# Performance work log

Hardware: AMD Instinct MI355X
Metric: run time of the kernel (lower is better)

The kernel has to match this reference:

```python
import jax, jax.numpy as jnp
import numpy as np

B, T, C, HEAD = 4, 4096, 1024, 64

def _rope_tables(t, d):
    # standard RoPE angles; each frequency repeated for the (even, odd) pair
    inv_freq = 1.0 / (10000.0 ** (np.arange(0, d, 2, dtype=np.float32) / d))  # (d/2,)
    ang = np.arange(t, dtype=np.float32)[:, None] * inv_freq[None, :]          # (t, d/2)
    ang = np.repeat(ang, 2, axis=-1)                                           # (t, d)
    return jnp.asarray(np.cos(ang)), jnp.asarray(np.sin(ang))

def setup_inputs() -> dict:
    key = jax.random.key(0)
    kx, kq, kk, kv = jax.random.split(key, 4)
    cos, sin = _rope_tables(T, HEAD)
    s = 1.0 / np.sqrt(C)
    return {
        "x": jax.random.normal(kx, (B, T, C), dtype=jnp.float32),
        "cos": cos,
        "sin": sin,
        "tril": jnp.tril(jnp.ones((T, T), dtype=jnp.int32)),
        "Wq": jax.random.normal(kq, (C, HEAD), dtype=jnp.float32) * s,
        "Wk": jax.random.normal(kk, (C, HEAD), dtype=jnp.float32) * s,
        "Wv": jax.random.normal(kv, (C, HEAD), dtype=jnp.float32) * s,
    }

def _apply_rope(x, cos, sin):
    # x: (B, T, D); cos/sin: (T, D)
    x1 = x[..., ::2]
    x2 = x[..., 1::2]
    rot = jnp.stack([-x2, x1], axis=-1).reshape(x.shape)
    return x * cos[None] + rot * sin[None]

def reference(x, cos, sin, tril, Wq, Wk, Wv):
    q = _apply_rope(x @ Wq, cos, sin)          # (B, T, D)
    k = _apply_rope(x @ Wk, cos, sin)          # (B, T, D)
    v = x @ Wv                                  # (B, T, D)
    scale = HEAD ** -0.5
    wei = jnp.einsum("btd,bsd->bts", q, k) * scale   # (B, T, T)
    wei = jnp.where(tril[None] == 0, -jnp.inf, wei)
    wei = jax.nn.softmax(wei, axis=-1)               # dropout p=0 (eval) -> identity
    return jnp.einsum("bts,bsd->btd", wei, v)        # (B, T, D)
```

## Files before the change

### kernel.cpp

```cpp
#include <hip/hip_runtime.h>
#include <math.h>

#define T_ 4096
#define NROWS 16384

typedef __attribute__((ext_vector_type(8))) short short8;
typedef __attribute__((ext_vector_type(4))) short short4v;
typedef __attribute__((ext_vector_type(4))) float float4v;
typedef __attribute__((ext_vector_type(2))) unsigned uint2v;

#define MFMA(a, b, c) __builtin_amdgcn_mfma_f32_16x16x32_bf16((a), (b), (c), 0, 0, 0)

#if defined(__has_builtin)
#if __has_builtin(__builtin_amdgcn_exp2f)
#define EXP2(x) __builtin_amdgcn_exp2f(x)
#else
#define EXP2(x) exp2f(x)
#endif
#else
#define EXP2(x) exp2f(x)
#endif

#define SCALE_Q 0.18033688011112042f

__device__ __forceinline__ short f2bf(float f) {
    unsigned u = __builtin_bit_cast(unsigned, f);
    u += 0x7fffu + ((u >> 16) & 1u);
    return (short)(u >> 16);
}
__device__ __forceinline__ float bf2f(short s) {
    return __builtin_bit_cast(float, ((unsigned)(unsigned short)s) << 16);
}
__device__ __forceinline__ unsigned pack_bf2(float a, float b) {
    unsigned ua = __builtin_bit_cast(unsigned, a);
    unsigned ub = __builtin_bit_cast(unsigned, b);
    ua += 0x7fffu + ((ua >> 16) & 1u);
    ub += 0x7fffu + ((ub >> 16) & 1u);
    return (ua >> 16) | (ub & 0xffff0000u);
}

__global__ void wprep_kernel(const float* __restrict__ Wq,
                             const float* __restrict__ Wk,
                             const float* __restrict__ Wv,
                             short* __restrict__ Wt2)
{
    const int ck = blockIdx.x;
    const int t = threadIdx.x;
    const int sub = t >> 6, lane = t & 63;
    const int ln = lane & 15, quad = lane >> 4;
#pragma unroll
    for (int jj = 0; jj < 3; ++jj) {
        const int nt = sub * 3 + jj;
        const float* W = (nt < 4) ? Wq : (nt < 8) ? Wk : Wv;
        const int col = (nt & 3) * 16 + ln;
        short8 o;
#pragma unroll
        for (int j = 0; j < 8; ++j)
            o[j] = f2bf(W[(size_t)(ck * 32 + quad * 8 + j) * 64 + col]);
        *(short8*)(Wt2 + ((size_t)(ck * 12 + nt) * 64 + lane) * 8) = o;
    }
}

__global__ __launch_bounds__(256, 2) void qkv_kernel(
    const float* __restrict__ x, const float* __restrict__ cosp,
    const float* __restrict__ sinp, const short* __restrict__ Wt2,
    short* __restrict__ Qb, short* __restrict__ Ks, short* __restrict__ Vs)
{
    __shared__ short4v MB[4][2][12][64];
    __shared__ short KT[32][72];

    const int t = threadIdx.x, w = t >> 6, lane = t & 63;
    const int ln = lane & 15, quad = lane >> 4;
    const int rb = blockIdx.x * 32;
    const int k0 = w * 256;

    const float* xp0 = x + (size_t)(rb + ln) * 1024 + k0 + quad * 8;
    const float* xp1 = x + (size_t)(rb + 16 + ln) * 1024 + k0 + quad * 8;
    const short* wp2 = Wt2 + ((size_t)(w * 8) * 12 * 64 + lane) * 8;

    short8 a[2][8];
#pragma unroll
    for (int af = 0; af < 2; ++af) {
        const float* xp = af ? xp1 : xp0;
        float4 xf[16];
#pragma unroll
        for (int it = 0; it < 8; ++it) {
            xf[it * 2]     = *(const float4*)(xp + it * 32);
            xf[it * 2 + 1] = *(const float4*)(xp + it * 32 + 4);
        }
#pragma unroll
        for (int it = 0; it < 8; ++it) {
            short8 v;
            v[0] = f2bf(xf[it * 2].x);     v[1] = f2bf(xf[it * 2].y);
            v[2] = f2bf(xf[it * 2].z);     v[3] = f2bf(xf[it * 2].w);
            v[4] = f2bf(xf[it * 2 + 1].x); v[5] = f2bf(xf[it * 2 + 1].y);
            v[6] = f2bf(xf[it * 2 + 1].z); v[7] = f2bf(xf[it * 2 + 1].w);
            a[af][it] = v;
        }
    }

    float4v acc[2][12];
#pragma unroll
    for (int af = 0; af < 2; ++af)
#pragma unroll
        for (int i = 0; i < 12; ++i) acc[af][i] = (float4v){0.f, 0.f, 0.f, 0.f};

#pragma unroll
    for (int it = 0; it < 8; ++it) {
        short8 bf[12];
#pragma unroll
        for (int nt = 0; nt < 12; ++nt)
            bf[nt] = *(const short8*)(wp2 + (size_t)(it * 12 + nt) * 512);
#pragma unroll
        for (int nt = 0; nt < 12; ++nt) {
            acc[0][nt] = MFMA(a[0][it], bf[nt], acc[0][nt]);
            acc[1][nt] = MFMA(a[1][it], bf[nt], acc[1][nt]);
        }
    }

#pragma unroll
    for (int af = 0; af < 2; ++af)
#pragma unroll
        for (int nt = 0; nt < 12; ++nt) {
            short4v pv;
#pragma unroll
            for (int reg = 0; reg < 4; ++reg) pv[reg] = f2bf(acc[af][nt][reg]);
            MB[w][af][nt][lane] = pv;
        }
    __syncthreads();

    const int b  = rb >> 12;
    const int kt = (rb & (T_ - 1)) >> 6;
#pragma unroll
    for (int af = 0; af < 2; ++af) {
        const int rb16 = rb + af * 16;
#pragma unroll
        for (int j = 0; j < 3; ++j) {
            const int nt = w * 3 + j;
            float m[4] = {0.f, 0.f, 0.f, 0.f};
#pragma unroll
            for (int p = 0; p < 4; ++p) {
                const short4v pv = MB[p][af][nt][lane];
#pragma unroll
                for (int reg = 0; reg < 4; ++reg) m[reg] += bf2f(pv[reg]);
            }
            if (nt < 4) {
                const int col = nt * 16 + ln;
#pragma unroll
                for (int reg = 0; reg < 4; ++reg) {
                    const int g  = rb16 + quad * 4 + reg;
                    const int tp = g & (T_ - 1);
                    const float cv = cosp[(size_t)tp * 64 + col];
                    const float sv = sinp[(size_t)tp * 64 + col];
                    const float v  = m[reg];
                    const float vp = __shfl_xor(v, 1, 64);
                    const float rot = (ln & 1) ? vp : -vp;
                    Qb[(size_t)g * 64 + col] = f2bf(fmaf(v, cv, rot * sv) * SCALE_Q);
                }
            } else if (nt < 8) {
                const int col = (nt & 3) * 16 + ln;
#pragma unroll
                for (int reg = 0; reg < 4; ++reg) {
                    const int g  = rb16 + quad * 4 + reg;
                    const int tp = g & (T_ - 1);
                    const float cv = cosp[(size_t)tp * 64 + col];
                    const float sv = sinp[(size_t)tp * 64 + col];
                    const float v  = m[reg];
                    const float vp = __shfl_xor(v, 1, 64);
                    const float rot = (ln & 1) ? vp : -vp;
                    KT[af * 16 + quad * 4 + reg][col] = f2bf(fmaf(v, cv, rot * sv));
                }
            } else {
                const int vnt = nt - 8;
                const int rowgrp = (rb16 >> 4) & 3;
                const int hh = rowgrp >> 1;
                const int qp = (rowgrp & 1) * 2 + (quad >> 1);
                const int jb = (quad & 1) * 4;
                short4v pv;
#pragma unroll
                for (int reg = 0; reg < 4; ++reg) pv[reg] = f2bf(m[reg]);
                const size_t addr =
                    ((((size_t)(b * 64 + kt) * 4 + vnt) * 2 + hh) * 64 + qp * 16 + ln) * 8 + jb;
                *(short4v*)(Vs + addr) = pv;
            }
        }
    }
    __syncthreads();

    {
        const int af2 = w >> 1, h2 = w & 1;
        const int st2 = ((rb >> 4) & 3) + af2;
        const short8 kfrag = *(const short8*)(&KT[af2 * 16 + ln][h2 * 32 + quad * 8]);
        *(short8*)(Ks + (((size_t)(b * 64 + kt) * 8 + st2 * 2 + h2) * 64 + lane) * 8) = kfrag;
    }
}

#define LOADK(kf, ktv)                                                         \
    {   const short* _kb = Ksp + (size_t)(ktv) * 4096 + lane * 8;              \
        _Pragma("unroll")                                                      \
        for (int u = 0; u < 8; ++u) kf[u] = *(const short8*)(_kb + u * 512); }

#define LOADV(vf, ktv)                                                         \
    {   const short* _vb = Vp + (size_t)(ktv) * 4096 + lane * 8;               \
        _Pragma("unroll")                                                      \
        for (int u = 0; u < 8; ++u) vf[u] = *(const short8*)(_vb + u * 512); }

#define CVTPK(dst, lo, hi)                                                     \
    asm("v_cvt_pk_bf16_f32 %0, %1, %2" : "=v"(dst) : "v"(lo), "v"(hi));

#define STEP(ktv, kf, vf, masked)                                              \
    {   float4v sA[4], sB[4];                                                  \
        __builtin_amdgcn_s_setprio(1);                                         \
        _Pragma("unroll")                                                      \
        for (int st = 0; st < 4; ++st) {                                       \
            sA[st] = (float4v){0.f, 0.f, 0.f, 0.f};                            \
            sA[st] = MFMA(kf[st * 2],     qA0, sA[st]);       \
            sA[st] = MFMA(kf[st * 2 + 1], qA1, sA[st]);                        \
            sB[st] = (float4v){0.f, 0.f, 0.f, 0.f};                            \
            sB[st] = MFMA(kf[st * 2],     qB0, sB[st]);                        \
            sB[st] = MFMA(kf[st * 2 + 1], qB1, sB[st]);                        \
        }                                                                      \
        __builtin_amdgcn_s_setprio(0);                                         \
        if (masked) {                                                          \
            _Pragma("unroll")                                                  \
            for (int st = 0; st < 4; ++st)                                     \
                _Pragma("unroll")                                              \
                for (int r = 0; r < 4; ++r) {                                  \
                    const int kc = (ktv) * 64 + st * 16 + quad * 4 + r;        \
                    if (kc > qr0 + ln)      sA[st][r] = -__builtin_inff();     \
                    if (kc > qr0 + 16 + ln) sB[st][r] = -__builtin_inff();     \
                }                                                              \
        }                                                                      \
        _Pragma("unroll")                                                      \
        for (int st = 0; st < 4; ++st)                                         \
            _Pragma("unroll")                                                  \
            for (int r = 0; r < 4; ++r) {                                      \
                const float pA = EXP2(sA[st][r]);                              \
                sA[st][r] = pA; lsumA += pA;                                   \
                const float pB = EXP2(sB[st][r]);                              \
                sB[st][r] = pB; lsumB += pB;                                   \
            }                                                                  \
        _Pragma("unroll")                                                      \
        for (int st = 0; st < 4; ++st) {                                       \
            uint2v pkA, pkB;                                                   \
            CVTPK(pkA[0], sA[st][0], sA[st][1])                                \
            CVTPK(pkA[1], sA[st][2], sA[st][3])                                \
            *(uint2v*)(pwA + ln * 104 + st * 16 + quad * 4) = pkA;             \
            CVTPK(pkB[0], sB[st][0], sB[st][1])                                \
            CVTPK(pkB[1], sB[st][2], sB[st][3])                                \
            *(uint2v*)(pwB + ln * 104 + st * 16 + quad * 4) = pkB;             \
        }                                                                      \
        const short8 aA0 = *(const short8*)(pwA + ln * 104 + quad * 8);        \
        const short8 aA1 = *(const short8*)(pwA + ln * 104 + quad * 8 + 32);   \
        const short8 aB0 = *(const short8*)(pwB + ln * 104 + quad * 8);        \
        const short8 aB1 = *(const short8*)(pwB + ln * 104 + quad * 8 + 32);   \
        __builtin_amdgcn_s_setprio(1);                                         \
        _Pragma("unroll")                                                      \
        for (int vn = 0; vn < 4; ++vn) {                                       \
            oA[vn] = MFMA(aA0, vf[vn * 2],     oA[vn]);                        \
            oA[vn] = MFMA(aA1, vf[vn * 2 + 1], oA[vn]);                        \
            oB[vn] = MFMA(aB0, vf[vn * 2],     oB[vn]);                        \
            oB[vn] = MFMA(aB1, vf[vn * 2 + 1], oB[vn]);                        \
        }                                                                      \
        __builtin_amdgcn_s_setprio(0);                                         \
    }

__global__ __launch_bounds__(512, 2) void attn_kernel(
    const short* __restrict__ Qb, const short* __restrict__ Ks,
    const short* __restrict__ Vs, float* __restrict__ out)
{
    __shared__ __align__(16) unsigned char smem[70656];
    short* const PLs = (short*)smem;
    float* const OLf = (float*)smem;
    float* const SLf = (float*)(smem + 69632);

    const int t = threadIdx.x, w = t >> 6, lane = t & 63;
    const int ln = lane & 15, quad = lane >> 4;
    const int bid = (int)blockIdx.x;
    const int b = bid >> 6;
    const int q = bid & 63;

    const short* Qp  = Qb + (size_t)b * T_ * 64;
    const short* Ksp = Ks + (size_t)b * T_ * 64;
    const short* Vp  = Vs + (size_t)b * T_ * 64;
    short* const pwA = PLs + (size_t)(w * 2) * 1664;
    short* const pwB = pwA + 1664;

    for (int job = 0; job < 2; ++job) {
        const int j   = job ? 127 - q : q;
        const int qr0 = j * 32;

        const short8 qA0 = *(const short8*)(Qp + (size_t)(qr0 + ln) * 64 + quad * 8);
        const short8 qA1 = *(const short8*)(Qp + (size_t)(qr0 + ln) * 64 + quad * 8 + 32);
        const short8 qB0 = *(const short8*)(Qp + (size_t)(qr0 + 16 + ln) * 64 + quad * 8);
        const short8 qB1 = *(const short8*)(Qp + (size_t)(qr0 + 16 + ln) * 64 + quad * 8 + 32);

        float lsumA = 0.f, lsumB = 0.f;
        float4v oA[4], oB[4];
#pragma unroll
        for (int i = 0; i < 4; ++i) {
            oA[i] = (float4v){0.f, 0.f, 0.f, 0.f};
            oB[i] = (float4v){0.f, 0.f, 0.f, 0.f};
        }

        const int ktend = j >> 1;
        short8 kfA[8], kfB[8], vf[8];

        int kt = w;
        if (kt <= ktend) {
            LOADK(kfA, kt)
            while (true) {
                {
                    const bool more = (kt + 8) <= ktend;
                    LOADV(vf, kt)
                    if (more) LOADK(kfB, kt + 8)
                    STEP(kt, kfA, vf, kt == ktend)
                    kt += 8;
                    if (!more) break;
                }
                {
                    const bool more = (kt + 8) <= ktend;
                    LOADV(vf, kt)
                    if (more) LOADK(kfA, kt + 8)
                    STEP(kt, kfB, vf, kt == ktend)
                    kt += 8;
                    if (!more) break;
                }
            }
        }

        lsumA += __shfl_xor(lsumA, 16, 64);
        lsumA += __shfl_xor(lsumA, 32, 64);
        lsumB += __shfl_xor(lsumB, 16, 64);
        lsumB += __shfl_xor(lsumB, 32, 64);

        __syncthreads();

#pragma unroll
        for (int vn = 0; vn < 4; ++vn)
#pragma unroll
            for (int r = 0; r < 4; ++r) {
                OLf[((size_t)w * 32 + quad * 4 + r) * 68 + vn * 16 + ln]      = oA[vn][r];
                OLf[((size_t)w * 32 + 16 + quad * 4 + r) * 68 + vn * 16 + ln] = oB[vn][r];
            }
        if (quad == 0) {
            SLf[w * 32 + ln]      = lsumA;
            SLf[w * 32 + 16 + ln] = lsumB;
        }
        __syncthreads();

        const int row = w * 4 + quad;
        float lstar = 0.f;
#pragma unroll
        for (int p = 0; p < 8; ++p) lstar += SLf[p * 32 + row];
        float ox = 0.f, oy = 0.f, oz = 0.f, ow_ = 0.f;
#pragma unroll
        for (int p = 0; p < 8; ++p) {
            const float4 ov = *(const float4*)&OLf[((size_t)p * 32 + row) * 68 + ln * 4];
            ox += ov.x; oy += ov.y; oz += ov.z; ow_ += ov.w;
        }
        const float inv = 1.f / lstar;
        float4 res; res.x = ox * inv; res.y = oy * inv; res.z = oz * inv; res.w = ow_ * inv;
        *(float4*)(out + ((size_t)b * T_ + qr0 + row) * 64 + ln * 4) = res;
        __syncthreads();
    }
}

extern "C" void kernel_launch(void* const* d_in, const int* in_sizes, int n_in,
                              void* d_out, int out_size, void* d_ws, size_t ws_size,
                              hipStream_t stream)
{
    const float* x    = (const float*)d_in[0];
    const float* cosp = (const float*)d_in[1];
    const float* sinp = (const float*)d_in[2];
    const float* Wq   = (const float*)d_in[4];
    const float* Wk   = (const float*)d_in[5];
    const float* Wv   = (const float*)d_in[6];
    float* out = (float*)d_out;

    short* Qb  = (short*)d_ws;
    short* Ks  = Qb + (size_t)NROWS * 64;
    short* Vs  = Ks + (size_t)NROWS * 64;
    short* Wt2 = Vs + (size_t)NROWS * 64;

    wprep_kernel<<<32, 256, 0, stream>>>(Wq, Wk, Wv, Wt2);
    qkv_kernel<<<NROWS / 32, 256, 0, stream>>>(x, cosp, sinp, Wt2, Qb, Ks, Vs);
    attn_kernel<<<256, 512, 0, stream>>>(Qb, Ks, Vs, out);
}
```

Measured before the change: 173.6 us.

## Software-pipeline attention loop: overlap PV of previous tile with QK softmax

Splits the per-tile step into a QK+softmax stage and a PV stage, then reorders the loop so the PV MFMAs of tile i run interleaved with the QK/softmax of tile i+1, using double-buffered P tiles in LDS and double-buffered V fragments. K prefetch double-buffering is replaced by a single K buffer loaded just before use. LDS grows to 106496 bytes, which may limit occupancy with 2 blocks per CU, and K load latency is no longer hidden by a full tile of prefetch.

```diff
diff --git a/kernel.cpp b/kernel.cpp
--- a/kernel.cpp
+++ b/kernel.cpp
@@ -30,13 +30,6 @@
 }
 __device__ __forceinline__ float bf2f(short s) {
     return __builtin_bit_cast(float, ((unsigned)(unsigned short)s) << 16);
-}
-__device__ __forceinline__ unsigned pack_bf2(float a, float b) {
-    unsigned ua = __builtin_bit_cast(unsigned, a);
-    unsigned ub = __builtin_bit_cast(unsigned, b);
-    ua += 0x7fffu + ((ua >> 16) & 1u);
-    ub += 0x7fffu + ((ub >> 16) & 1u);
-    return (ua >> 16) | (ub & 0xffff0000u);
 }
 
 __global__ void wprep_kernel(const float* __restrict__ Wq,
@@ -208,7 +201,7 @@
 #define CVTPK(dst, lo, hi)                                                     \
     asm("v_cvt_pk_bf16_f32 %0, %1, %2" : "=v"(dst) : "v"(lo), "v"(hi));
 
-#define STEP(ktv, kf, vf, masked)                                              \
+#define QKSOFT(ktv, pa, pb, masked)                                            \
     {   float4v sA[4], sB[4];                                                  \
         __builtin_amdgcn_s_setprio(1);                                         \
         _Pragma("unroll")                                                      \
@@ -245,22 +238,25 @@
             uint2v pkA, pkB;                                                   \
             CVTPK(pkA[0], sA[st][0], sA[st][1])                                \
             CVTPK(pkA[1], sA[st][2], sA[st][3])                                \
-            *(uint2v*)(pwA + ln * 104 + st * 16 + quad * 4) = pkA;             \
+            *(uint2v*)((pa) + ln * 104 + st * 16 + quad * 4) = pkA;            \
             CVTPK(pkB[0], sB[st][0], sB[st][1])                                \
             CVTPK(pkB[1], sB[st][2], sB[st][3])                                \
-            *(uint2v*)(pwB + ln * 104 + st * 16 + quad * 4) = pkB;             \
+            *(uint2v*)((pb) + ln * 104 + st * 16 + quad * 4) = pkB;            \
         }                                                                      \
-        const short8 aA0 = *(const short8*)(pwA + ln * 104 + quad * 8);        \
-        const short8 aA1 = *(const short8*)(pwA + ln * 104 + quad * 8 + 32);   \
-        const short8 aB0 = *(const short8*)(pwB + ln * 104 + quad * 8);        \
-        const short8 aB1 = *(const short8*)(pwB + ln * 104 + quad * 8 + 32);   \
+    }
+
+#define PVSTEP(pa, pb, vv)                                                     \
+    {   const short8 aA0 = *(const short8*)((pa) + ln * 104 + quad * 8);       \
+        const short8 aA1 = *(const short8*)((pa) + ln * 104 + quad * 8 + 32);  \
+        const short8 aB0 = *(const short8*)((pb) + ln * 104 + quad * 8);       \
+        const short8 aB1 = *(const short8*)((pb) + ln * 104 + quad * 8 + 32);  \
         __builtin_amdgcn_s_setprio(1);                                         \
         _Pragma("unroll")                                                      \
         for (int vn = 0; vn < 4; ++vn) {                                       \
-            oA[vn] = MFMA(aA0, vf[vn * 2],     oA[vn]);                        \
-            oA[vn] = MFMA(aA1, vf[vn * 2 + 1], oA[vn]);                        \
-            oB[vn] = MFMA(aB0, vf[vn * 2],     oB[vn]);                        \
-            oB[vn] = MFMA(aB1, vf[vn * 2 + 1], oB[vn]);                        \
+            oA[vn] = MFMA(aA0, vv[vn * 2],     oA[vn]);                        \
+            oA[vn] = MFMA(aA1, vv[vn * 2 + 1], oA[vn]);                        \
+            oB[vn] = MFMA(aB0, vv[vn * 2],     oB[vn]);                        \
+            oB[vn] = MFMA(aB1, vv[vn * 2 + 1], oB[vn]);                        \
         }                                                                      \
         __builtin_amdgcn_s_setprio(0);                                         \
     }
@@ -269,7 +265,7 @@
     const short* __restrict__ Qb, const short* __restrict__ Ks,
     const short* __restrict__ Vs, float* __restrict__ out)
 {
-    __shared__ __align__(16) unsigned char smem[70656];
+    __shared__ __align__(16) unsigned char smem[106496];
     short* const PLs = (short*)smem;
     float* const OLf = (float*)smem;
     float* const SLf = (float*)(smem + 69632);
@@ -283,8 +279,11 @@
     const short* Qp  = Qb + (size_t)b * T_ * 64;
     const short* Ksp = Ks + (size_t)b * T_ * 64;
     const short* Vp  = Vs + (size_t)b * T_ * 64;
-    short* const pwA = PLs + (size_t)(w * 2) * 1664;
-    short* const pwB = pwA + 1664;
+    short* const pw  = PLs + (size_t)w * 6656;
+    short* const p0A = pw;
+    short* const p0B = pw + 1664;
+    short* const p1A = pw + 3328;
+    short* const p1B = pw + 4992;
 
     for (int job = 0; job < 2; ++job) {
         const int j   = job ? 127 - q : q;
@@ -304,28 +303,27 @@
         }
 
         const int ktend = j >> 1;
-        short8 kfA[8], kfB[8], vf[8];
+        short8 kf[8], vf0[8], vf1[8];
 
         int kt = w;
         if (kt <= ktend) {
-            LOADK(kfA, kt)
+            LOADK(kf, kt)
+            LOADV(vf0, kt)
+            QKSOFT(kt, p0A, p0B, kt == ktend)
+            kt += 8;
             while (true) {
-                {
-                    const bool more = (kt + 8) <= ktend;
-                    LOADV(vf, kt)
-                    if (more) LOADK(kfB, kt + 8)
-                    STEP(kt, kfA, vf, kt == ktend)
-                    kt += 8;
-                    if (!more) break;
-                }
-                {
-                    const bool more = (kt + 8) <= ktend;
-                    LOADV(vf, kt)
-                    if (more) LOADK(kfA, kt + 8)
-                    STEP(kt, kfB, vf, kt == ktend)
-                    kt += 8;
-                    if (!more) break;
-                }
+                if (kt > ktend) { PVSTEP(p0A, p0B, vf0) break; }
+                LOADK(kf, kt)
+                LOADV(vf1, kt)
+                PVSTEP(p0A, p0B, vf0)
+                QKSOFT(kt, p1A, p1B, kt == ktend)
+                kt += 8;
+                if (kt > ktend) { PVSTEP(p1A, p1B, vf1) break; }
+                LOADK(kf, kt)
+                LOADV(vf0, kt)
+                PVSTEP(p1A, p1B, vf1)
+                QKSOFT(kt, p0A, p0B, kt == ktend)
+                kt += 8;
             }
         }
 
```

New measurement: 172.5 us, median of 2. About the same (-0.7%).
